# Kernel optimization log

Hardware: AMD Instinct MI355X
Metric: run time of the kernel (lower is better)

## Reference

```python
import jax, jax.numpy as jnp
import numpy as np

N = 50000   # nodes
E = 800000  # edges (avg degree 16)
FIN = 128   # input node features
H = 4       # heads (conv1, conv2)
C = 64      # hidden_channels (per-head out dim)
SLOPE = 0.2
LN_EPS = 1e-5


def gatv2(x, src, dst, Wl, bl, Wr, br, att, bo, heads, outc, n):
    # GATv2Conv: e = att . LeakyReLU(x_l[src] + x_r[dst]); segment-softmax over dst; scatter-add alpha * x_l[src]
    xl = (x @ Wl + bl).reshape(n, heads, outc)
    xr = (x @ Wr + br).reshape(n, heads, outc)
    e = jax.nn.leaky_relu(xl[src] + xr[dst], SLOPE)          # [E, H, C]
    score = jnp.einsum('ehc,hc->eh', e, att)                 # [E, H]
    smax = jax.ops.segment_max(score, dst, num_segments=n)   # [N, H]
    ex = jnp.exp(score - smax[dst])
    denom = jax.ops.segment_sum(ex, dst, num_segments=n)
    alpha = ex / (denom[dst] + 1e-16)                        # [E, H]
    out = jax.ops.segment_sum(alpha[:, :, None] * xl[src], dst, num_segments=n)  # [N, H, C]
    return out.reshape(n, heads * outc) + bo                 # concat=True (default)


def layernorm(x, g, b):
    mu = x.mean(-1, keepdims=True)
    var = ((x - mu) ** 2).mean(-1, keepdims=True)
    return (x - mu) * jax.lax.rsqrt(var + LN_EPS) * g + b


def setup_inputs() -> dict:
    key = jax.random.key(0)
    ks = jax.random.split(key, 32)
    f32 = jnp.float32
    def nrm(k, shape, s):
        return jax.random.normal(k, shape, dtype=f32) * s
    inp = {}
    inp['x'] = jax.random.normal(ks[0], (N, FIN), dtype=f32)
    inp['edge_index'] = jax.random.randint(ks[1], (2, E), 0, N, dtype=jnp.int32)
    inp['batch'] = jnp.zeros((N,), dtype=jnp.int32)
    # conv1: 128 -> 4*64
    inp['W1l'] = nrm(ks[2], (FIN, H * C), 1.0 / np.sqrt(FIN))
    inp['b1l'] = jnp.zeros((H * C,), f32)
    inp['W1r'] = nrm(ks[3], (FIN, H * C), 1.0 / np.sqrt(FIN))
    inp['b1r'] = jnp.zeros((H * C,), f32)
    inp['a1'] = nrm(ks[4], (H, C), 1.0 / np.sqrt(C))
    inp['bo1'] = jnp.zeros((H * C,), f32)
    inp['ln1_g'] = jnp.ones((H * C,), f32)
    inp['ln1_b'] = jnp.zeros((H * C,), f32)
    # conv2: 256 -> 4*64
    inp['W2l'] = nrm(ks[5], (H * C, H * C), 1.0 / np.sqrt(H * C))
    inp['b2l'] = jnp.zeros((H * C,), f32)
    inp['W2r'] = nrm(ks[6], (H * C, H * C), 1.0 / np.sqrt(H * C))
    inp['b2r'] = jnp.zeros((H * C,), f32)
    inp['a2'] = nrm(ks[7], (H, C), 1.0 / np.sqrt(C))
    inp['bo2'] = jnp.zeros((H * C,), f32)
    inp['ln2_g'] = jnp.ones((H * C,), f32)
    inp['ln2_b'] = jnp.zeros((H * C,), f32)
    # conv3: 256 -> 1*64 (heads=1)
    inp['W3l'] = nrm(ks[8], (H * C, C), 1.0 / np.sqrt(H * C))
    inp['b3l'] = jnp.zeros((C,), f32)
    inp['W3r'] = nrm(ks[9], (H * C, C), 1.0 / np.sqrt(H * C))
    inp['b3r'] = jnp.zeros((C,), f32)
    inp['a3'] = nrm(ks[10], (1, C), 1.0 / np.sqrt(C))
    inp['bo3'] = jnp.zeros((C,), f32)
    inp['ln3_g'] = jnp.ones((C,), f32)
    inp['ln3_b'] = jnp.zeros((C,), f32)
    # final linear 64 -> 64
    inp['linW'] = nrm(ks[11], (C, C), 1.0 / np.sqrt(C))
    inp['linb'] = jnp.zeros((C,), f32)
    return inp


def reference(x, edge_index, batch,
              W1l, b1l, W1r, b1r, a1, bo1, ln1_g, ln1_b,
              W2l, b2l, W2r, b2r, a2, bo2, ln2_g, ln2_b,
              W3l, b3l, W3r, b3r, a3, bo3, ln3_g, ln3_b,
              linW, linb):
    src, dst = edge_index[0], edge_index[1]
    n = x.shape[0]
    h = gatv2(x, src, dst, W1l, b1l, W1r, b1r, a1, bo1, H, C, n)
    h = layernorm(h, ln1_g, ln1_b)
    h = gatv2(h, src, dst, W2l, b2l, W2r, b2r, a2, bo2, H, C, n)
    h = layernorm(h, ln2_g, ln2_b)
    h = gatv2(h, src, dst, W3l, b3l, W3r, b3r, a3, bo3, 1, C, n)
    h = layernorm(h, ln3_g, ln3_b)
    return h @ linW + linb
```

## Files before the change

kernel.cpp:

```cpp
#include <hip/hip_runtime.h>
#include <math.h>

#define LRELU_SLOPE 0.2f
#define L2E 1.4426950408889634f

typedef __attribute__((ext_vector_type(8))) short bf16x8;
typedef __attribute__((ext_vector_type(4))) float f32x4;
typedef __attribute__((ext_vector_type(2))) float f2;

__device__ __forceinline__ float fast_exp2(float x) {
  float r; asm("v_exp_f32 %0, %1" : "=v"(r) : "v"(x)); return r;
}

__device__ __forceinline__ unsigned short f2bf(float f) {
  unsigned u = __float_as_uint(f);
  return (unsigned short)((u + 0x7FFFu + ((u >> 16) & 1u)) >> 16);
}
__device__ __forceinline__ f2 bfpair(unsigned p) {
  f2 r;
  r.x = __uint_as_float(p << 16);
  r.y = __uint_as_float(p & 0xffff0000u);
  return r;
}

__global__ void cvt_bf16(const float* __restrict__ in, unsigned short* __restrict__ out, int n4) {
  int i = blockIdx.x * blockDim.x + threadIdx.x;
  if (i >= n4) return;
  float4 v = *(const float4*)(in + (size_t)i * 4);
  ushort4 o;
  o.x = f2bf(v.x); o.y = f2bf(v.y); o.z = f2bf(v.z); o.w = f2bf(v.w);
  *(ushort4*)(out + (size_t)i * 4) = o;
}

__global__ void wt_cvt_all(
    const float* __restrict__ W1l, const float* __restrict__ W1r,
    const float* __restrict__ W2l, const float* __restrict__ W2r,
    const float* __restrict__ W3l, const float* __restrict__ W3r,
    unsigned short* __restrict__ Wt1l, unsigned short* __restrict__ Wt1r,
    unsigned short* __restrict__ Wt2l, unsigned short* __restrict__ Wt2r,
    unsigned short* __restrict__ Wt3l, unsigned short* __restrict__ Wt3r) {
  const float* W; unsigned short* Wt; int K, N;
  switch (blockIdx.y) {
    case 0: W = W1l; Wt = Wt1l; K = 128; N = 256; break;
    case 1: W = W1r; Wt = Wt1r; K = 128; N = 256; break;
    case 2: W = W2l; Wt = Wt2l; K = 256; N = 256; break;
    case 3: W = W2r; Wt = Wt2r; K = 256; N = 256; break;
    case 4: W = W3l; Wt = Wt3l; K = 256; N = 64;  break;
    default: W = W3r; Wt = Wt3r; K = 256; N = 64; break;
  }
  int i = blockIdx.x * blockDim.x + threadIdx.x;
  int k8s = K / 8;
  int n = i / k8s, k8 = i - n * k8s;
  if (n >= N) return;
  unsigned short tmp[8];
#pragma unroll
  for (int j = 0; j < 8; ++j) tmp[j] = f2bf(W[(size_t)(k8 * 8 + j) * N + n]);
  *(bf16x8*)(Wt + (size_t)n * K + k8 * 8) = *(bf16x8*)tmp;
}

template<int K, int RT>
__global__ __launch_bounds__(256) void gemm_mfma2(
    const unsigned short* __restrict__ Xb,
    const unsigned short* __restrict__ Wt0, const unsigned short* __restrict__ Wt1,
    const float* __restrict__ bias0, const float* __restrict__ bias1,
    unsigned short* __restrict__ Y0, unsigned short* __restrict__ Y1, int M, int N) {
  const int nblk = N >> 6;
  const int side = blockIdx.y / nblk;
  const int n0 = (blockIdx.y - side * nblk) * 64;
  const unsigned short* Wt = side ? Wt1 : Wt0;
  const float* bias = side ? bias1 : bias0;
  unsigned short* Y = side ? Y1 : Y0;

  const int t = threadIdx.x, w = t >> 6, l = t & 63;
  const int lr = l & 15, lk = l >> 4;
  const int rowBase = blockIdx.x * (RT * 64) + w * (RT * 16);

  f32x4 acc[RT][4];
#pragma unroll
  for (int rt = 0; rt < RT; ++rt)
#pragma unroll
    for (int nt = 0; nt < 4; ++nt) acc[rt][nt] = (f32x4){0.f, 0.f, 0.f, 0.f};

  const unsigned short* ap[RT];
#pragma unroll
  for (int rt = 0; rt < RT; ++rt) {
    int row = rowBase + rt * 16 + lr;
    if (row >= M) row = M - 1;
    ap[rt] = Xb + (size_t)row * K + lk * 8;
  }
  const unsigned short* bp = Wt + (size_t)(n0 + lr) * K + lk * 8;

#pragma unroll
  for (int k0 = 0; k0 < K; k0 += 32) {
    bf16x8 a[RT], b[4];
#pragma unroll
    for (int rt = 0; rt < RT; ++rt) a[rt] = *(const bf16x8*)(ap[rt] + k0);
#pragma unroll
    for (int nt = 0; nt < 4; ++nt) b[nt] = *(const bf16x8*)(bp + (size_t)nt * 16 * K + k0);
#pragma unroll
    for (int rt = 0; rt < RT; ++rt)
#pragma unroll
      for (int nt = 0; nt < 4; ++nt)
        acc[rt][nt] = __builtin_amdgcn_mfma_f32_16x16x32_bf16(a[rt], b[nt], acc[rt][nt], 0, 0, 0);
  }

#pragma unroll
  for (int nt = 0; nt < 4; ++nt) {
    float bv = bias[n0 + nt * 16 + lr];
#pragma unroll
    for (int rt = 0; rt < RT; ++rt) {
#pragma unroll
      for (int r = 0; r < 4; ++r) {
        int row = rowBase + rt * 16 + lk * 4 + r;
        if (row < M) Y[(size_t)row * N + n0 + nt * 16 + lr] = f2bf(acc[rt][nt][r] + bv);
      }
    }
  }
}

__global__ void hist_deg(const int* __restrict__ dst, int* __restrict__ deg, int Ee) {
  int e = blockIdx.x * blockDim.x + threadIdx.x;
  if (e < Ee) atomicAdd(&deg[dst[e]], 1);
}

__global__ void scan_blk(const int* __restrict__ deg, int* __restrict__ rowptr,
                         int* __restrict__ bsum, int n) {
  __shared__ int sm[256];
  const int b = blockIdx.x, t = threadIdx.x;
  const int i = b * 256 + t;
  const int v = (i < n) ? deg[i] : 0;
  sm[t] = v;
  __syncthreads();
#pragma unroll
  for (int off = 1; off < 256; off <<= 1) {
    int x = (t >= off) ? sm[t - off] : 0;
    __syncthreads();
    sm[t] += x;
    __syncthreads();
  }
  if (i < n) rowptr[i] = sm[t] - v;
  if (t == 255) bsum[b] = sm[255];
}

__global__ void scan_top(const int* __restrict__ bsum, int* __restrict__ boff,
                         int* __restrict__ rowptr, int nb, int n) {
  __shared__ int sm[1024];
  const int t = threadIdx.x;
  const int v = (t < nb) ? bsum[t] : 0;
  sm[t] = v;
  __syncthreads();
#pragma unroll
  for (int off = 1; off < 1024; off <<= 1) {
    int x = (t >= off) ? sm[t - off] : 0;
    __syncthreads();
    sm[t] += x;
    __syncthreads();
  }
  if (t < nb) boff[t] = sm[t] - v;
  if (t == 1023) rowptr[n] = sm[1023];
}

__global__ void scan_add(int* __restrict__ rowptr, const int* __restrict__ boff, int n) {
  int i = blockIdx.x * 256 + threadIdx.x;
  if (i < n) rowptr[i] += boff[blockIdx.x];
}

__global__ void fill_csr(const int* __restrict__ src, const int* __restrict__ dst,
                         const int* __restrict__ rowptr, int* __restrict__ deg,
                         int* __restrict__ csr_src, int Ee) {
  int e = blockIdx.x * blockDim.x + threadIdx.x;
  if (e >= Ee) return;
  int d = dst[e];
  int p = atomicSub(&deg[d], 1) - 1;
  csr_src[rowptr[d] + p] = src[e];
}

__global__ __launch_bounds__(256) void gat_fused4(
    const unsigned short* __restrict__ xlb, const unsigned short* __restrict__ xrb,
    const float* __restrict__ att,
    const int* __restrict__ rowptr, const int* __restrict__ csr_src,
    const float* __restrict__ bo, const float* __restrict__ gam,
    const float* __restrict__ bet, unsigned short* __restrict__ outp, int n) {
  const int t = threadIdx.x;
  const int wv = t >> 6, lane = t & 63;
  const int node = blockIdx.x * 4 + wv;
  if (node >= n) return;
  const int cb = lane * 4;

  uint2 xp = *(const uint2*)(xrb + (size_t)node * 256 + cb);
  const f2 xr0 = bfpair(xp.x), xr1 = bfpair(xp.y);
  const float4 a4 = *(const float4*)(att + cb);
  const f2 at0 = {a4.x * L2E, a4.y * L2E};
  const f2 at1 = {a4.z * L2E, a4.w * L2E};

  const int r0 = rowptr[node], r1 = rowptr[node + 1];
  float s = 0.f;
  f2 o0 = {0.f, 0.f}, o1 = {0.f, 0.f};

  if (r0 < r1) {
    const int last = r1 - 1;
    uint2 p0 = *(const uint2*)(xlb + (size_t)csr_src[r0] * 256 + cb);
    uint2 p1 = *(const uint2*)(xlb + (size_t)csr_src[min(r0 + 1, last)] * 256 + cb);
    uint2 p2 = *(const uint2*)(xlb + (size_t)csr_src[min(r0 + 2, last)] * 256 + cb);
    uint2 p3 = *(const uint2*)(xlb + (size_t)csr_src[min(r0 + 3, last)] * 256 + cb);
    for (int i = r0; i < r1; i += 4) {
      const uint2 c0 = p0, c1 = p1, c2 = p2, c3 = p3;
      if (i + 4 < r1) {
        p0 = *(const uint2*)(xlb + (size_t)csr_src[min(i + 4, last)] * 256 + cb);
        p1 = *(const uint2*)(xlb + (size_t)csr_src[min(i + 5, last)] * 256 + cb);
        p2 = *(const uint2*)(xlb + (size_t)csr_src[min(i + 6, last)] * 256 + cb);
        p3 = *(const uint2*)(xlb + (size_t)csr_src[min(i + 7, last)] * 256 + cb);
      }
      const f2 v00 = bfpair(c0.x), v01 = bfpair(c0.y);
      const f2 v10 = bfpair(c1.x), v11 = bfpair(c1.y);
      const f2 v20 = bfpair(c2.x), v21 = bfpair(c2.y);
      const f2 v30 = bfpair(c3.x), v31 = bfpair(c3.y);

      f2 e;
      f2 q0, q1, q2, q3;
      e = v00 + xr0; e = __builtin_elementwise_max(e, e * LRELU_SLOPE); q0 = e * at0;
      e = v01 + xr1; e = __builtin_elementwise_max(e, e * LRELU_SLOPE); q0 += e * at1;
      e = v10 + xr0; e = __builtin_elementwise_max(e, e * LRELU_SLOPE); q1 = e * at0;
      e = v11 + xr1; e = __builtin_elementwise_max(e, e * LRELU_SLOPE); q1 += e * at1;
      e = v20 + xr0; e = __builtin_elementwise_max(e, e * LRELU_SLOPE); q2 = e * at0;
      e = v21 + xr1; e = __builtin_elementwise_max(e, e * LRELU_SLOPE); q2 += e * at1;
      e = v30 + xr0; e = __builtin_elementwise_max(e, e * LRELU_SLOPE); q3 = e * at0;
      e = v31 + xr1; e = __builtin_elementwise_max(e, e * LRELU_SLOPE); q3 += e * at1;

      float s0 = q0.x + q0.y, s1 = q1.x + q1.y, s2 = q2.x + q2.y, s3 = q3.x + q3.y;
      s0 += __shfl_xor(s0, 1); s1 += __shfl_xor(s1, 1);
      s2 += __shfl_xor(s2, 1); s3 += __shfl_xor(s3, 1);
      s0 += __shfl_xor(s0, 2); s1 += __shfl_xor(s1, 2);
      s2 += __shfl_xor(s2, 2); s3 += __shfl_xor(s3, 2);
      s0 += __shfl_xor(s0, 4); s1 += __shfl_xor(s1, 4);
      s2 += __shfl_xor(s2, 4); s3 += __shfl_xor(s3, 4);
      s0 += __shfl_xor(s0, 8); s1 += __shfl_xor(s1, 8);
      s2 += __shfl_xor(s2, 8); s3 += __shfl_xor(s3, 8);
      if (i + 1 >= r1) s1 = -INFINITY;
      if (i + 2 >= r1) s2 = -INFINITY;
      if (i + 3 >= r1) s3 = -INFINITY;
      const float w0 = fast_exp2(s0), w1 = fast_exp2(s1);
      const float w2 = fast_exp2(s2), w3 = fast_exp2(s3);
      s += (w0 + w1) + (w2 + w3);
      o0 += v00 * w0; o1 += v01 * w0;
      o0 += v10 * w1; o1 += v11 * w1;
      o0 += v20 * w2; o1 += v21 * w2;
      o0 += v30 * w3; o1 += v31 * w3;
    }
  }

  const float inv = 1.f / (s + 1e-16f);
  const float4 b4 = *(const float4*)(bo + cb);
  const float v0 = fmaf(o0.x, inv, b4.x);
  const float v1 = fmaf(o0.y, inv, b4.y);
  const float v2 = fmaf(o1.x, inv, b4.z);
  const float v3 = fmaf(o1.y, inv, b4.w);

  float ls = v0 + v1 + v2 + v3;
#pragma unroll
  for (int off = 1; off < 64; off <<= 1) ls += __shfl_xor(ls, off);
  const float mu = ls * (1.f / 256.f);
  const float d0 = v0 - mu, d1 = v1 - mu, d2 = v2 - mu, d3 = v3 - mu;
  float q = d0 * d0 + d1 * d1 + d2 * d2 + d3 * d3;
#pragma unroll
  for (int off = 1; off < 64; off <<= 1) q += __shfl_xor(q, off);
  const float rs = rsqrtf(q * (1.f / 256.f) + 1e-5f);

  const float4 g4 = *(const float4*)(gam + cb);
  const float4 e4 = *(const float4*)(bet + cb);
  ushort4 res;
  res.x = f2bf(fmaf(d0 * rs, g4.x, e4.x));
  res.y = f2bf(fmaf(d1 * rs, g4.y, e4.y));
  res.z = f2bf(fmaf(d2 * rs, g4.z, e4.z));
  res.w = f2bf(fmaf(d3 * rs, g4.w, e4.w));
  *(ushort4*)(outp + (size_t)node * 256 + cb) = res;
}

__global__ __launch_bounds__(512) void gat1_lin(
    const unsigned short* __restrict__ xlb, const unsigned short* __restrict__ xrb,
    const float* __restrict__ att,
    const int* __restrict__ rowptr, const int* __restrict__ csr_src,
    const float* __restrict__ bo, const float* __restrict__ gam,
    const float* __restrict__ bet,
    const float* __restrict__ linW, const float* __restrict__ linb,
    float* __restrict__ outp, int n) {
  const int OUT = 64;
  const int t = threadIdx.x;
  const int wv = t >> 6, lane = t & 63;
  const int grp = lane >> 3, c8 = lane & 7;
  __shared__ float lw[64][64];
  __shared__ float hbuf[8][64];
  for (int i = t; i < 4096; i += 512) lw[i >> 6][i & 63] = linW[i];

  const int node = blockIdx.x * 8 + wv;
  const bool active = node < n;
  const int cb = c8 * 8;

  f2 xr2[4];
  int r0 = 0, r1 = 0;
  if (active) {
    uint4 p = *(const uint4*)(xrb + (size_t)node * OUT + cb);
    xr2[0] = bfpair(p.x); xr2[1] = bfpair(p.y); xr2[2] = bfpair(p.z); xr2[3] = bfpair(p.w);
    r0 = rowptr[node];
    r1 = rowptr[node + 1];
  } else {
#pragma unroll
    for (int j = 0; j < 4; ++j) xr2[j] = (f2){0.f, 0.f};
  }
  f2 at2[4];
  {
    float4 a0 = *(const float4*)(att + cb);
    float4 a1 = *(const float4*)(att + cb + 4);
    at2[0] = (f2){a0.x * L2E, a0.y * L2E}; at2[1] = (f2){a0.z * L2E, a0.w * L2E};
    at2[2] = (f2){a1.x * L2E, a1.y * L2E}; at2[3] = (f2){a1.z * L2E, a1.w * L2E};
  }

  float s = 0.f;
  f2 o2[4];
#pragma unroll
  for (int j = 0; j < 4; ++j) o2[j] = (f2){0.f, 0.f};

  uint4 vpk = {0u, 0u, 0u, 0u};
  {
    int i0 = r0 + grp;
    if (i0 < r1) vpk = *(const uint4*)(xlb + (size_t)csr_src[i0] * OUT + cb);
  }
  bool valid = (r0 + grp) < r1;

  for (int base = r0; base < r1; base += 8) {
    const uint4 pc = vpk;
    const bool vld = valid;
    int inext = base + 8 + grp;
    valid = inext < r1;
    if (valid) vpk = *(const uint4*)(xlb + (size_t)csr_src[inext] * OUT + cb);

    f2 v0 = bfpair(pc.x), v1 = bfpair(pc.y), v2 = bfpair(pc.z), v3 = bfpair(pc.w);
    f2 e0 = v0 + xr2[0]; e0 = __builtin_elementwise_max(e0, e0 * LRELU_SLOPE);
    f2 e1 = v1 + xr2[1]; e1 = __builtin_elementwise_max(e1, e1 * LRELU_SLOPE);
    f2 e2 = v2 + xr2[2]; e2 = __builtin_elementwise_max(e2, e2 * LRELU_SLOPE);
    f2 e3 = v3 + xr2[3]; e3 = __builtin_elementwise_max(e3, e3 * LRELU_SLOPE);
    f2 sc2 = e0 * at2[0];
    sc2 += e1 * at2[1];
    sc2 += e2 * at2[2];
    sc2 += e3 * at2[3];
    float sc = sc2.x + sc2.y;
    sc += __shfl_xor(sc, 1);
    sc += __shfl_xor(sc, 2);
    sc += __shfl_xor(sc, 4);
    if (!vld) sc = -INFINITY;
    const float w = fast_exp2(sc);
    s += w;
    o2[0] += v0 * w;
    o2[1] += v1 * w;
    o2[2] += v2 * w;
    o2[3] += v3 * w;
  }

  float o[8] = {o2[0].x, o2[0].y, o2[1].x, o2[1].y, o2[2].x, o2[2].y, o2[3].x, o2[3].y};
#pragma unroll
  for (int off = 8; off < 64; off <<= 1) {
#pragma unroll
    for (int i = 0; i < 8; ++i) o[i] += __shfl_xor(o[i], off);
    s += __shfl_xor(s, off);
  }

  const float inv = 1.f / (s + 1e-16f);
  float val[8];
  {
    float4 b0 = *(const float4*)(bo + cb);
    float4 b1 = *(const float4*)(bo + cb + 4);
    val[0] = fmaf(o[0], inv, b0.x); val[1] = fmaf(o[1], inv, b0.y);
    val[2] = fmaf(o[2], inv, b0.z); val[3] = fmaf(o[3], inv, b0.w);
    val[4] = fmaf(o[4], inv, b1.x); val[5] = fmaf(o[5], inv, b1.y);
    val[6] = fmaf(o[6], inv, b1.z); val[7] = fmaf(o[7], inv, b1.w);
  }

  float ls = 0.f;
#pragma unroll
  for (int i = 0; i < 8; ++i) ls += val[i];
  ls += __shfl_xor(ls, 1);
  ls += __shfl_xor(ls, 2);
  ls += __shfl_xor(ls, 4);
  float mu = ls * (1.f / 64.f);
  float d[8], q = 0.f;
#pragma unroll
  for (int i = 0; i < 8; ++i) { d[i] = val[i] - mu; q = fmaf(d[i], d[i], q); }
  q += __shfl_xor(q, 1);
  q += __shfl_xor(q, 2);
  q += __shfl_xor(q, 4);
  float var = q * (1.f / 64.f);
  const float rs = rsqrtf(var + 1e-5f);

  if (grp == 0) {
    float4 g0 = *(const float4*)(gam + cb);
    float4 g1 = *(const float4*)(gam + cb + 4);
    float4 e0 = *(const float4*)(bet + cb);
    float4 e1 = *(const float4*)(bet + cb + 4);
    float* hb = &hbuf[wv][cb];
    hb[0] = fmaf(d[0] * rs, g0.x, e0.x); hb[1] = fmaf(d[1] * rs, g0.y, e0.y);
    hb[2] = fmaf(d[2] * rs, g0.z, e0.z); hb[3] = fmaf(d[3] * rs, g0.w, e0.w);
    hb[4] = fmaf(d[4] * rs, g1.x, e1.x); hb[5] = fmaf(d[5] * rs, g1.y, e1.y);
    hb[6] = fmaf(d[6] * rs, g1.z, e1.z); hb[7] = fmaf(d[7] * rs, g1.w, e1.w);
  }
  __syncthreads();

  float acc = linb[lane];
#pragma unroll 8
  for (int k = 0; k < 64; ++k) acc = fmaf(hbuf[wv][k], lw[k][lane], acc);
  if (active) outp[(size_t)node * 64 + lane] = acc;
}

extern "C" void kernel_launch(void* const* d_in, const int* in_sizes, int n_in,
                              void* d_out, int out_size, void* d_ws, size_t ws_size,
                              hipStream_t stream) {
  const float* x    = (const float*)d_in[0];
  const int*   eidx = (const int*)d_in[1];
  const int Nn = in_sizes[0] / 128;
  const int Ee = in_sizes[1] / 2;
  const int* src = eidx;
  const int* dst = eidx + Ee;

  const float* W1l = (const float*)d_in[3];  const float* b1l = (const float*)d_in[4];
  const float* W1r = (const float*)d_in[5];  const float* b1r = (const float*)d_in[6];
  const float* a1  = (const float*)d_in[7];  const float* bo1 = (const float*)d_in[8];
  const float* g1  = (const float*)d_in[9];  const float* be1 = (const float*)d_in[10];
  const float* W2l = (const float*)d_in[11]; const float* b2l = (const float*)d_in[12];
  const float* W2r = (const float*)d_in[13]; const float* b2r = (const float*)d_in[14];
  const float* a2  = (const float*)d_in[15]; const float* bo2 = (const float*)d_in[16];
  const float* g2  = (const float*)d_in[17]; const float* be2 = (const float*)d_in[18];
  const float* W3l = (const float*)d_in[19]; const float* b3l = (const float*)d_in[20];
  const float* W3r = (const float*)d_in[21]; const float* b3r = (const float*)d_in[22];
  const float* a3  = (const float*)d_in[23]; const float* bo3 = (const float*)d_in[24];
  const float* g3  = (const float*)d_in[25]; const float* be3 = (const float*)d_in[26];
  const float* linW = (const float*)d_in[27]; const float* linb = (const float*)d_in[28];

  char* ws = (char*)d_ws;
  unsigned short* xl   = (unsigned short*)ws; ws += (size_t)Nn * 256 * 2;
  unsigned short* xr   = (unsigned short*)ws; ws += (size_t)Nn * 256 * 2;
  unsigned short* Xb   = (unsigned short*)ws; ws += (size_t)Nn * 256 * 2;
  unsigned short* Wt1l = (unsigned short*)ws; ws += 256 * 128 * 2;
  unsigned short* Wt1r = (unsigned short*)ws; ws += 256 * 128 * 2;
  unsigned short* Wt2l = (unsigned short*)ws; ws += 256 * 256 * 2;
  unsigned short* Wt2r = (unsigned short*)ws; ws += 256 * 256 * 2;
  unsigned short* Wt3l = (unsigned short*)ws; ws += 64 * 256 * 2;
  unsigned short* Wt3r = (unsigned short*)ws; ws += 64 * 256 * 2;
  int*   deg    = (int*)ws;    ws += (size_t)Nn * 4;
  int*   rowptr = (int*)ws;    ws += (size_t)(Nn + 1) * 4;
  int*   bsum   = (int*)ws;    ws += 1024 * 4;
  int*   boff   = (int*)ws;    ws += 1024 * 4;
  int*   csr_src= (int*)ws;    ws += (size_t)Ee * 4;

  const int eblk = (Ee + 255) / 256;
  const int nblk = (Nn + 255) / 256;

  hipMemsetAsync(deg, 0, (size_t)Nn * 4, stream);
  hist_deg<<<eblk, 256, 0, stream>>>(dst, deg, Ee);
  wt_cvt_all<<<dim3(32, 6), 256, 0, stream>>>(W1l, W1r, W2l, W2r, W3l, W3r,
                                              Wt1l, Wt1r, Wt2l, Wt2r, Wt3l, Wt3r);
  scan_blk<<<nblk, 256, 0, stream>>>(deg, rowptr, bsum, Nn);
  scan_top<<<1, 1024, 0, stream>>>(bsum, boff, rowptr, nblk, Nn);
  scan_add<<<nblk, 256, 0, stream>>>(rowptr, boff, Nn);
  fill_csr<<<eblk, 256, 0, stream>>>(src, dst, rowptr, deg, csr_src, Ee);

  cvt_bf16<<<(Nn * 128 / 4 + 255) / 256, 256, 0, stream>>>(x, Xb, Nn * 128 / 4);
  gemm_mfma2<128, 4><<<dim3((Nn + 255) / 256, 8), 256, 0, stream>>>(
      Xb, Wt1l, Wt1r, b1l, b1r, xl, xr, Nn, 256);
  gat_fused4<<<(Nn + 3) / 4, 256, 0, stream>>>(xl, xr, a1, rowptr, csr_src, bo1, g1, be1, Xb, Nn);

  gemm_mfma2<256, 4><<<dim3((Nn + 255) / 256, 8), 256, 0, stream>>>(
      Xb, Wt2l, Wt2r, b2l, b2r, xl, xr, Nn, 256);
  gat_fused4<<<(Nn + 3) / 4, 256, 0, stream>>>(xl, xr, a2, rowptr, csr_src, bo2, g2, be2, Xb, Nn);

  gemm_mfma2<256, 1><<<dim3((Nn + 63) / 64, 2), 256, 0, stream>>>(
      Xb, Wt3l, Wt3r, b3l, b3r, xl, xr, Nn, 64);
  gat1_lin<<<(Nn + 7) / 8, 512, 0, stream>>>(xl, xr, a3, rowptr, csr_src, bo3, g3, be3,
                                             linW, linb, (float*)d_out, Nn);
}
```

Before: 462.7 us.

## Add LDS-staged dual-output GEMM sharing activation tile across both weight sides

Adds a gemm_dual kernel in which a 512-thread block stages a 64-row activation tile in shared memory once. Its eight waves then compute all 256 columns of both the left and right projections from that tile, replacing the old grid where each block reread the activations from global memory per 64-column slice and side. The change cuts redundant activation reads for conv1 and conv2. The costs are fewer, larger blocks, a large accumulator set per wave that may raise register pressure, and weights still read straight from global memory.

```diff
diff --git a/kernel.cpp b/kernel.cpp
--- a/kernel.cpp
+++ b/kernel.cpp
@@ -56,6 +56,72 @@
 #pragma unroll
   for (int j = 0; j < 8; ++j) tmp[j] = f2bf(W[(size_t)(k8 * 8 + j) * N + n]);
   *(bf16x8*)(Wt + (size_t)n * K + k8 * 8) = *(bf16x8*)tmp;
+}
+
+template<int K>
+__global__ __launch_bounds__(512) void gemm_dual(
+    const unsigned short* __restrict__ Xb,
+    const unsigned short* __restrict__ Wt0, const unsigned short* __restrict__ Wt1,
+    const float* __restrict__ bias0, const float* __restrict__ bias1,
+    unsigned short* __restrict__ Y0, unsigned short* __restrict__ Y1, int M) {
+  constexpr int LDK = K + 8;
+  __shared__ unsigned short As[64 * LDK];
+  const int t = threadIdx.x, w = t >> 6, l = t & 63;
+  const int lr = l & 15, lk = l >> 4;
+  const int rowBase = blockIdx.x * 64;
+
+  constexpr int SPR = K / 8;
+  constexpr int ITER = (64 * SPR) / 512;
+#pragma unroll
+  for (int i = 0; i < ITER; ++i) {
+    int idx = i * 512 + t;
+    int row = idx / SPR, seg = idx - row * SPR;
+    int gr = rowBase + row; if (gr >= M) gr = M - 1;
+    *(uint4*)(As + row * LDK + seg * 8) = *(const uint4*)(Xb + (size_t)gr * K + seg * 8);
+  }
+  __syncthreads();
+
+  const int side = w >> 2;
+  const int n0 = (w & 3) * 64;
+  const unsigned short* Wt = side ? Wt1 : Wt0;
+  const float* bias = side ? bias1 : bias0;
+  unsigned short* Y = side ? Y1 : Y0;
+
+  f32x4 acc[4][4];
+#pragma unroll
+  for (int rt = 0; rt < 4; ++rt)
+#pragma unroll
+    for (int nt = 0; nt < 4; ++nt) acc[rt][nt] = (f32x4){0.f, 0.f, 0.f, 0.f};
+
+  const unsigned short* bp = Wt + (size_t)(n0 + lr) * K + lk * 8;
+  const unsigned short* ap = As + lr * LDK + lk * 8;
+
+#pragma unroll
+  for (int k0 = 0; k0 < K; k0 += 32) {
+    bf16x8 a[4], b[4];
+#pragma unroll
+    for (int rt = 0; rt < 4; ++rt) a[rt] = *(const bf16x8*)(ap + rt * 16 * LDK + k0);
+#pragma unroll
+    for (int nt = 0; nt < 4; ++nt) b[nt] = *(const bf16x8*)(bp + nt * 16 * K + k0);
+#pragma unroll
+    for (int rt = 0; rt < 4; ++rt)
+#pragma unroll
+      for (int nt = 0; nt < 4; ++nt)
+        acc[rt][nt] = __builtin_amdgcn_mfma_f32_16x16x32_bf16(a[rt], b[nt], acc[rt][nt], 0, 0, 0);
+  }
+
+#pragma unroll
+  for (int nt = 0; nt < 4; ++nt) {
+    float bv = bias[n0 + nt * 16 + lr];
+#pragma unroll
+    for (int rt = 0; rt < 4; ++rt) {
+#pragma unroll
+      for (int r = 0; r < 4; ++r) {
+        int row = rowBase + rt * 16 + lk * 4 + r;
+        if (row < M) Y[(size_t)row * 256 + n0 + nt * 16 + lr] = f2bf(acc[rt][nt][r] + bv);
+      }
+    }
+  }
 }
 
 template<int K, int RT>
@@ -462,13 +528,13 @@
   scan_add<<<nblk, 256, 0, stream>>>(rowptr, boff, Nn);
   fill_csr<<<eblk, 256, 0, stream>>>(src, dst, rowptr, deg, csr_src, Ee);
 
+  const int gdblk = (Nn + 63) / 64;
+
   cvt_bf16<<<(Nn * 128 / 4 + 255) / 256, 256, 0, stream>>>(x, Xb, Nn * 128 / 4);
-  gemm_mfma2<128, 4><<<dim3((Nn + 255) / 256, 8), 256, 0, stream>>>(
-      Xb, Wt1l, Wt1r, b1l, b1r, xl, xr, Nn, 256);
+  gemm_dual<128><<<gdblk, 512, 0, stream>>>(Xb, Wt1l, Wt1r, b1l, b1r, xl, xr, Nn);
   gat_fused4<<<(Nn + 3) / 4, 256, 0, stream>>>(xl, xr, a1, rowptr, csr_src, bo1, g1, be1, Xb, Nn);
 
-  gemm_mfma2<256, 4><<<dim3((Nn + 255) / 256, 8), 256, 0, stream>>>(
-      Xb, Wt2l, Wt2r, b2l, b2r, xl, xr, Nn, 256);
+  gemm_dual<256><<<gdblk, 512, 0, stream>>>(Xb, Wt2l, Wt2r, b2l, b2r, xl, xr, Nn);
   gat_fused4<<<(Nn + 3) / 4, 256, 0, stream>>>(xl, xr, a2, rowptr, csr_src, bo2, g2, be2, Xb, Nn);
 
   gemm_mfma2<256, 1><<<dim3((Nn + 63) / 64, 2), 256, 0, stream>>>(
```

Measured after the change: 453.5 us. -2.0%, faster.
